# Performance work log

Measured on AMD Instinct MI355X. Metric: run time of the kernel, lower is better.

Reference implementation:

```python
import jax, jax.numpy as jnp
import numpy as np

NUM_HEADS = 12
QK_SCALE = 1.0
EPS = 1e-12  # torch.nn.functional.normalize default eps


def _l2norm(t):
    # matches torch F.normalize: x / max(||x||_2, eps) along last axis
    n = jnp.sqrt(jnp.sum(t * t, axis=-1, keepdims=True))
    return t / jnp.maximum(n, EPS)


def setup_inputs() -> dict:
    key = jax.random.key(0)
    k1, k2 = jax.random.split(key)
    B, N, dim = 8, 4096, 768
    x = jax.random.normal(k1, (B, N, 3 * dim), dtype=jnp.float32)
    temperature = jnp.ones((NUM_HEADS, 1, 1), dtype=jnp.float32)
    proj_w = jax.random.normal(k2, (dim, dim), dtype=jnp.float32) * (1.0 / np.sqrt(dim))
    proj_b = jnp.zeros((dim,), dtype=jnp.float32)
    return {"x": x, "temperature": temperature, "proj_w": proj_w, "proj_b": proj_b}


def reference(x, temperature, proj_w, proj_b):
    B, N, C3 = x.shape
    C = C3 // 3
    H = NUM_HEADS
    d = C // H
    # (B, N, 3, H, d) -> (3, B, H, N, d)
    qkv = x.reshape(B, N, 3, H, d).transpose(2, 0, 3, 1, 4)
    q, k, v = qkv[0], qkv[1], qkv[2]
    q = jnp.swapaxes(q, -2, -1) * QK_SCALE   # [B, H, d, N]
    v = jnp.swapaxes(v, -2, -1)              # [B, H, d, N]
    q = _l2norm(q)                           # normalize over tokens N
    k = _l2norm(k)                           # normalize over head dim d (k is [B,H,N,d])
    # cross-covariance attention over channels: [B, H, d, d]
    attn = jnp.einsum('bhdn,bhne->bhde', q, k) * temperature
    attn = jax.nn.softmax(attn, axis=-1)
    out = jnp.einsum('bhde,bhen->bhdn', attn, v)  # [B, H, d, N]
    out = out.transpose(0, 3, 1, 2).reshape(B, N, C)  # [B, N, C]
    out = out @ proj_w.T + proj_b
    return out
```

## Files before the change

kernel.cpp:

```cpp
#include <hip/hip_runtime.h>
#include <hip/hip_bf16.h>

#define BB 8
#define NN 4096
#define HH 12
#define CC 768
#define C3 2304

typedef float  f32x4  __attribute__((ext_vector_type(4)));
typedef __bf16 bf16x8 __attribute__((ext_vector_type(8)));
typedef __bf16 bf16x4 __attribute__((ext_vector_type(4)));

__device__ __forceinline__ void gload16(const void* g, void* l) {
  __builtin_amdgcn_global_load_lds((const __attribute__((address_space(1))) void*)g,
                                   (__attribute__((address_space(3))) void*)l, 16, 0, 0);
}

__global__ __launch_bounds__(256) void k1_logits(const float* __restrict__ x,
                                                 __bf16* __restrict__ vb,
                                                 float* __restrict__ Spart,
                                                 float* __restrict__ Qpart) {
  const int slice = blockIdx.x;
  const int h = blockIdx.y, b = blockIdx.z;
  const int tid = threadIdx.x;
  __shared__ __bf16 qT[2][64][40];
  __shared__ __bf16 kT[2][64][40];
  __shared__ float  qws[4][64];

  const int t   = tid >> 3;
  const int sub = tid & 7;
  const int w   = tid >> 6, lane = tid & 63;
  const int fr  = lane & 15, fk = lane >> 4;
  const int c0  = sub * 8;

  const float* qbase = x + (size_t)(b * NN + slice * 256) * C3 + h * 64 + c0;

  float qss8[8];
#pragma unroll
  for (int j = 0; j < 8; ++j) qss8[j] = 0.f;
  f32x4 acc[4];
#pragma unroll
  for (int tn = 0; tn < 4; ++tn) acc[tn] = (f32x4){0.f, 0.f, 0.f, 0.f};

  {
    const float* qp = qbase + (size_t)t * C3;
    const float4 q0 = *(const float4*)(qp);
    const float4 q1 = *(const float4*)(qp + 4);
    const float4 k0 = *(const float4*)(qp + 768);
    const float4 k1 = *(const float4*)(qp + 772);
    float ss = k0.x * k0.x + k0.y * k0.y + k0.z * k0.z + k0.w * k0.w +
               k1.x * k1.x + k1.y * k1.y + k1.z * k1.z + k1.w * k1.w;
    ss += __shfl_xor(ss, 1);
    ss += __shfl_xor(ss, 2);
    ss += __shfl_xor(ss, 4);
    const float inv = 1.0f / fmaxf(sqrtf(ss), 1e-12f);
    qT[0][c0 + 0][t] = (__bf16)q0.x; qT[0][c0 + 1][t] = (__bf16)q0.y;
    qT[0][c0 + 2][t] = (__bf16)q0.z; qT[0][c0 + 3][t] = (__bf16)q0.w;
    qT[0][c0 + 4][t] = (__bf16)q1.x; qT[0][c0 + 5][t] = (__bf16)q1.y;
    qT[0][c0 + 6][t] = (__bf16)q1.z; qT[0][c0 + 7][t] = (__bf16)q1.w;
    kT[0][c0 + 0][t] = (__bf16)(k0.x * inv); kT[0][c0 + 1][t] = (__bf16)(k0.y * inv);
    kT[0][c0 + 2][t] = (__bf16)(k0.z * inv); kT[0][c0 + 3][t] = (__bf16)(k0.w * inv);
    kT[0][c0 + 4][t] = (__bf16)(k1.x * inv); kT[0][c0 + 5][t] = (__bf16)(k1.y * inv);
    kT[0][c0 + 6][t] = (__bf16)(k1.z * inv); kT[0][c0 + 7][t] = (__bf16)(k1.w * inv);
    qss8[0] = fmaf(q0.x, q0.x, qss8[0]); qss8[1] = fmaf(q0.y, q0.y, qss8[1]);
    qss8[2] = fmaf(q0.z, q0.z, qss8[2]); qss8[3] = fmaf(q0.w, q0.w, qss8[3]);
    qss8[4] = fmaf(q1.x, q1.x, qss8[4]); qss8[5] = fmaf(q1.y, q1.y, qss8[5]);
    qss8[6] = fmaf(q1.z, q1.z, qss8[6]); qss8[7] = fmaf(q1.w, q1.w, qss8[7]);
  }
  __syncthreads();

#pragma unroll
  for (int step = 0; step < 8; ++step) {
    const int cur = step & 1;
    float4 q0, q1, k0, k1;
    if (step < 7) {
      const float* np = qbase + (size_t)((step + 1) * 32 + t) * C3;
      q0 = *(const float4*)(np);
      q1 = *(const float4*)(np + 4);
      k0 = *(const float4*)(np + 768);
      k1 = *(const float4*)(np + 772);
    }
    const bf16x8 afr = *(const bf16x8*)&qT[cur][w * 16 + fr][fk * 8];
    const bf16x8 b0 = *(const bf16x8*)&kT[cur][0 * 16 + fr][fk * 8];
    const bf16x8 b1 = *(const bf16x8*)&kT[cur][1 * 16 + fr][fk * 8];
    const bf16x8 b2 = *(const bf16x8*)&kT[cur][2 * 16 + fr][fk * 8];
    const bf16x8 b3 = *(const bf16x8*)&kT[cur][3 * 16 + fr][fk * 8];
    acc[0] = __builtin_amdgcn_mfma_f32_16x16x32_bf16(afr, b0, acc[0], 0, 0, 0);
    acc[1] = __builtin_amdgcn_mfma_f32_16x16x32_bf16(afr, b1, acc[1], 0, 0, 0);
    acc[2] = __builtin_amdgcn_mfma_f32_16x16x32_bf16(afr, b2, acc[2], 0, 0, 0);
    acc[3] = __builtin_amdgcn_mfma_f32_16x16x32_bf16(afr, b3, acc[3], 0, 0, 0);
    if (step < 7) {
      const int nxt = cur ^ 1;
      float ss = k0.x * k0.x + k0.y * k0.y + k0.z * k0.z + k0.w * k0.w +
                 k1.x * k1.x + k1.y * k1.y + k1.z * k1.z + k1.w * k1.w;
      ss += __shfl_xor(ss, 1);
      ss += __shfl_xor(ss, 2);
      ss += __shfl_xor(ss, 4);
      const float inv = 1.0f / fmaxf(sqrtf(ss), 1e-12f);
      qT[nxt][c0 + 0][t] = (__bf16)q0.x; qT[nxt][c0 + 1][t] = (__bf16)q0.y;
      qT[nxt][c0 + 2][t] = (__bf16)q0.z; qT[nxt][c0 + 3][t] = (__bf16)q0.w;
      qT[nxt][c0 + 4][t] = (__bf16)q1.x; qT[nxt][c0 + 5][t] = (__bf16)q1.y;
      qT[nxt][c0 + 6][t] = (__bf16)q1.z; qT[nxt][c0 + 7][t] = (__bf16)q1.w;
      kT[nxt][c0 + 0][t] = (__bf16)(k0.x * inv); kT[nxt][c0 + 1][t] = (__bf16)(k0.y * inv);
      kT[nxt][c0 + 2][t] = (__bf16)(k0.z * inv); kT[nxt][c0 + 3][t] = (__bf16)(k0.w * inv);
      kT[nxt][c0 + 4][t] = (__bf16)(k1.x * inv); kT[nxt][c0 + 5][t] = (__bf16)(k1.y * inv);
      kT[nxt][c0 + 6][t] = (__bf16)(k1.z * inv); kT[nxt][c0 + 7][t] = (__bf16)(k1.w * inv);
      qss8[0] = fmaf(q0.x, q0.x, qss8[0]); qss8[1] = fmaf(q0.y, q0.y, qss8[1]);
      qss8[2] = fmaf(q0.z, q0.z, qss8[2]); qss8[3] = fmaf(q0.w, q0.w, qss8[3]);
      qss8[4] = fmaf(q1.x, q1.x, qss8[4]); qss8[5] = fmaf(q1.y, q1.y, qss8[5]);
      qss8[6] = fmaf(q1.z, q1.z, qss8[6]); qss8[7] = fmaf(q1.w, q1.w, qss8[7]);
    }
    __syncthreads();
  }

  const int bh = b * HH + h;
  float* Sp = Spart + ((size_t)(slice * 96 + bh)) * 4096;
#pragma unroll
  for (int tn = 0; tn < 4; ++tn)
#pragma unroll
    for (int rr = 0; rr < 4; ++rr)
      Sp[(w * 16 + fk * 4 + rr) * 64 + tn * 16 + fr] = acc[tn][rr];

#pragma unroll
  for (int j = 0; j < 8; ++j) {
    float v = qss8[j];
    v += __shfl_xor(v, 8);
    v += __shfl_xor(v, 16);
    v += __shfl_xor(v, 32);
    if (lane < 8) qws[w][lane * 8 + j] = v;
  }
  __syncthreads();
  if (tid < 64) {
    const float qs = qws[0][tid] + qws[1][tid] + qws[2][tid] + qws[3][tid];
    Qpart[((size_t)(slice * 96 + bh)) * 64 + tid] = qs;
  }

  const float* vsrc = x + (size_t)(b * NN + slice * 256) * C3 + 1536 + h * 64 + c0;
  __bf16* vdst = vb + (size_t)(b * NN + slice * 256) * CC + h * 64 + c0;
#pragma unroll
  for (int r = 0; r < 8; ++r) {
    const size_t tok = (size_t)(r * 32 + t);
    const float4 v0 = *(const float4*)(vsrc + tok * C3);
    const float4 v1 = *(const float4*)(vsrc + tok * C3 + 4);
    bf16x8 vv;
    vv[0] = (__bf16)v0.x; vv[1] = (__bf16)v0.y; vv[2] = (__bf16)v0.z; vv[3] = (__bf16)v0.w;
    vv[4] = (__bf16)v1.x; vv[5] = (__bf16)v1.y; vv[6] = (__bf16)v1.z; vv[7] = (__bf16)v1.w;
    *(bf16x8*)(vdst + tok * CC) = vv;
  }
}

__global__ __launch_bounds__(512) void k2_softmax(const float* __restrict__ Spart,
                                                  const float* __restrict__ Qpart,
                                                  const float* __restrict__ temp,
                                                  float* __restrict__ attn) {
  const int h = blockIdx.x, b = blockIdx.y;
  const int tid = threadIdx.x;
  const int i = tid >> 3;
  const int g = tid & 7;
  const int bh = b * HH + h;
  float qs = 0.f;
#pragma unroll
  for (int s = 0; s < 16; ++s) qs += Qpart[((size_t)(s * 96 + bh)) * 64 + i];
  float v[8];
#pragma unroll
  for (int j = 0; j < 8; ++j) v[j] = 0.f;
#pragma unroll 4
  for (int s = 0; s < 16; ++s) {
    const float* Sp = Spart + ((size_t)(s * 96 + bh)) * 4096 + i * 64 + g * 8;
    const float4 t0 = *(const float4*)(Sp);
    const float4 t1 = *(const float4*)(Sp + 4);
    v[0] += t0.x; v[1] += t0.y; v[2] += t0.z; v[3] += t0.w;
    v[4] += t1.x; v[5] += t1.y; v[6] += t1.z; v[7] += t1.w;
  }
  const float rqs = 1.0f / fmaxf(sqrtf(qs), 1e-12f);
  const float tp  = temp[h] * rqs;
  float m = -3.4e38f;
#pragma unroll
  for (int j = 0; j < 8; ++j) { v[j] *= tp; m = fmaxf(m, v[j]); }
  m = fmaxf(m, __shfl_xor(m, 1));
  m = fmaxf(m, __shfl_xor(m, 2));
  m = fmaxf(m, __shfl_xor(m, 4));
  float s = 0.f;
#pragma unroll
  for (int j = 0; j < 8; ++j) { v[j] = __expf(v[j] - m); s += v[j]; }
  s += __shfl_xor(s, 1);
  s += __shfl_xor(s, 2);
  s += __shfl_xor(s, 4);
  const float inv = 1.0f / s;
  float* Ap = attn + (size_t)bh * 4096 + i * 64 + g * 8;
  float4 o0, o1;
  o0.x = v[0] * inv; o0.y = v[1] * inv; o0.z = v[2] * inv; o0.w = v[3] * inv;
  o1.x = v[4] * inv; o1.y = v[5] * inv; o1.z = v[6] * inv; o1.w = v[7] * inv;
  *(float4*)(Ap)     = o0;
  *(float4*)(Ap + 4) = o1;
}

__global__ __launch_bounds__(256) void k3_w2(const float* __restrict__ attn,
                                             const float* __restrict__ pw,
                                             __bf16* __restrict__ W2) {
  const int ct = blockIdx.x, h = blockIdx.y, b = blockIdx.z;
  const int co0 = ct * 64;
  __shared__ float pT[64][65];
  __shared__ float ab[64][64];
  const int tid = threadIdx.x;
  const int r = tid >> 2, c0 = (tid & 3) * 16;
  {
    const float* pp = pw + (size_t)(co0 + r) * CC + h * 64 + c0;
    const float4 p0 = *(const float4*)(pp + 0);
    const float4 p1 = *(const float4*)(pp + 4);
    const float4 p2 = *(const float4*)(pp + 8);
    const float4 p3 = *(const float4*)(pp + 12);
    const float* ap = attn + (size_t)(b * HH + h) * 4096 + r * 64 + c0;
    const float4 a0 = *(const float4*)(ap + 0);
    const float4 a1 = *(const float4*)(ap + 4);
    const float4 a2 = *(const float4*)(ap + 8);
    const float4 a3 = *(const float4*)(ap + 12);
    pT[c0 +  0][r] = p0.x; pT[c0 +  1][r] = p0.y; pT[c0 +  2][r] = p0.z; pT[c0 +  3][r] = p0.w;
    pT[c0 +  4][r] = p1.x; pT[c0 +  5][r] = p1.y; pT[c0 +  6][r] = p1.z; pT[c0 +  7][r] = p1.w;
    pT[c0 +  8][r] = p2.x; pT[c0 +  9][r] = p2.y; pT[c0 + 10][r] = p2.z; pT[c0 + 11][r] = p2.w;
    pT[c0 + 12][r] = p3.x; pT[c0 + 13][r] = p3.y; pT[c0 + 14][r] = p3.z; pT[c0 + 15][r] = p3.w;
    *(float4*)&ab[r][c0 + 0]  = a0;
    *(float4*)&ab[r][c0 + 4]  = a1;
    *(float4*)&ab[r][c0 + 8]  = a2;
    *(float4*)&ab[r][c0 + 12] = a3;
  }
  __syncthreads();
  const int col = tid & 63, jg = tid >> 6;
  float accJ[16];
#pragma unroll
  for (int c = 0; c < 16; ++c) accJ[c] = 0.f;
#pragma unroll 4
  for (int i = 0; i < 64; ++i) {
    const float p = pT[i][col];
    const float4* a4 = (const float4*)&ab[i][jg * 16];
    const float4 A0 = a4[0], A1 = a4[1], A2 = a4[2], A3 = a4[3];
    accJ[0]  = fmaf(p, A0.x, accJ[0]);  accJ[1]  = fmaf(p, A0.y, accJ[1]);
    accJ[2]  = fmaf(p, A0.z, accJ[2]);  accJ[3]  = fmaf(p, A0.w, accJ[3]);
    accJ[4]  = fmaf(p, A1.x, accJ[4]);  accJ[5]  = fmaf(p, A1.y, accJ[5]);
    accJ[6]  = fmaf(p, A1.z, accJ[6]);  accJ[7]  = fmaf(p, A1.w, accJ[7]);
    accJ[8]  = fmaf(p, A2.x, accJ[8]);  accJ[9]  = fmaf(p, A2.y, accJ[9]);
    accJ[10] = fmaf(p, A2.z, accJ[10]); accJ[11] = fmaf(p, A2.w, accJ[11]);
    accJ[12] = fmaf(p, A3.x, accJ[12]); accJ[13] = fmaf(p, A3.y, accJ[13]);
    accJ[14] = fmaf(p, A3.z, accJ[14]); accJ[15] = fmaf(p, A3.w, accJ[15]);
  }
  bf16x8 u0, u1;
#pragma unroll
  for (int c = 0; c < 8; ++c) { u0[c] = (__bf16)accJ[c]; u1[c] = (__bf16)accJ[8 + c]; }
  __bf16* wp = W2 + ((size_t)b * CC + co0 + col) * CC + h * 64 + jg * 16;
  *(bf16x8*)(wp)     = u0;
  *(bf16x8*)(wp + 8) = u1;
}

__global__ __launch_bounds__(256) void k4_gemm(const __bf16* __restrict__ vb,
                                               const __bf16* __restrict__ W2,
                                               const float* __restrict__ pb,
                                               float* __restrict__ out) {
  int id = blockIdx.x;
  const int bz = id / 192;
  const int rem = id - bz * 192;
  const int mg = rem / 48;
  const int idx = rem - mg * 48;
  const int nt = idx >> 3;
  const int mt = mg * 8 + (idx & 7);
  const int m0 = mt * 128, co0 = nt * 128;

  __shared__ __bf16 At[128][32];
  __shared__ __bf16 Bt[128][32];

  const int tid  = threadIdx.x;
  const int w    = tid >> 6, lane = tid & 63;
  const int wm   = w >> 1,   wn   = w & 1;
  const int fr   = lane & 15;
  const int fk   = lane >> 4;

  f32x4 acc[4][4];
#pragma unroll
  for (int tm = 0; tm < 4; ++tm)
#pragma unroll
    for (int tn = 0; tn < 4; ++tn) acc[tm][tn] = (f32x4){0.f, 0.f, 0.f, 0.f};

  const int srow = lane >> 2;
  const int scol = (lane & 3) * 8;
  const __bf16* Ag = vb + (size_t)(bz * NN + m0 + w * 32 + srow) * CC + scol;
  const __bf16* Bg = W2 + ((size_t)bz * CC + co0 + w * 32 + srow) * CC + scol;
  __bf16* lA0 = &At[w * 32][0];
  __bf16* lA1 = &At[w * 32 + 16][0];
  __bf16* lB0 = &Bt[w * 32][0];
  __bf16* lB1 = &Bt[w * 32 + 16][0];

  for (int kk = 0; kk < 24; ++kk) {
    const int kb = kk * 32;
    __syncthreads();
    gload16(Ag + kb,            lA0);
    gload16(Ag + 16 * CC + kb,  lA1);
    gload16(Bg + kb,            lB0);
    gload16(Bg + 16 * CC + kb,  lB1);
    __syncthreads();
    bf16x8 afr[4], bfr[4];
#pragma unroll
    for (int tm = 0; tm < 4; ++tm)
      afr[tm] = *(const bf16x8*)&At[wm * 64 + tm * 16 + fr][fk * 8];
#pragma unroll
    for (int tn = 0; tn < 4; ++tn)
      bfr[tn] = *(const bf16x8*)&Bt[wn * 64 + tn * 16 + fr][fk * 8];
#pragma unroll
    for (int tm = 0; tm < 4; ++tm)
#pragma unroll
      for (int tn = 0; tn < 4; ++tn)
        acc[tm][tn] = __builtin_amdgcn_mfma_f32_16x16x32_bf16(afr[tm], bfr[tn],
                                                              acc[tm][tn], 0, 0, 0);
  }

#pragma unroll
  for (int tn = 0; tn < 4; ++tn) {
    const int co = co0 + wn * 64 + tn * 16 + fr;
    const float bias = pb[co];
#pragma unroll
    for (int tm = 0; tm < 4; ++tm) {
#pragma unroll
      for (int rr = 0; rr < 4; ++rr) {
        const int row = m0 + wm * 64 + tm * 16 + fk * 4 + rr;
        out[(size_t)(bz * NN + row) * CC + co] = acc[tm][tn][rr] + bias;
      }
    }
  }
}

extern "C" void kernel_launch(void* const* d_in, const int* in_sizes, int n_in,
                              void* d_out, int out_size, void* d_ws, size_t ws_size,
                              hipStream_t stream) {
  const float* x    = (const float*)d_in[0];
  const float* temp = (const float*)d_in[1];
  const float* pw   = (const float*)d_in[2];
  const float* pb   = (const float*)d_in[3];
  float* out = (float*)d_out;
  char* ws = (char*)d_ws;

  float*  Spart = (float*)(ws);
  float*  Qpart = (float*)(ws + 25165824);
  float*  attn  = (float*)(ws + 25559040);
  __bf16* W2    = (__bf16*)(ws + 27131904);
  __bf16* vb    = (__bf16*)(ws + 36569088);

  hipLaunchKernelGGL(k1_logits,  dim3(16, 12, 8), dim3(256), 0, stream, x, vb, Spart, Qpart);
  hipLaunchKernelGGL(k2_softmax, dim3(12, 8),     dim3(512), 0, stream, Spart, Qpart, temp, attn);
  hipLaunchKernelGGL(k3_w2,      dim3(12, 12, 8), dim3(256), 0, stream, attn, pw, W2);
  hipLaunchKernelGGL(k4_gemm,    dim3(1536),      dim3(256), 0, stream, vb, W2, pb, out);
}
```

Baseline: 521.9 us.

## Fuse V fp32-to-bf16 conversion into GEMM A-tile load, drop vb buffer

Removes the V conversion pass from the logits kernel and the intermediate bf16 V buffer. The final GEMM now reads V directly from the fp32 input, converts it to bf16 in registers and stores it to LDS, with the next tile's loads issued early as register prefetch. The block index is also remapped so consecutive blocks land on different batches (an XCD-style swizzle). This saves a write and a re-read of the bf16 intermediate. In exchange the GEMM reads fp32 (twice the bytes) and in-kernel register staging replaces the async global-to-LDS path for A.

```diff
diff --git a/kernel.cpp b/kernel.cpp
--- a/kernel.cpp
+++ b/kernel.cpp
@@ -17,7 +17,6 @@
 }
 
 __global__ __launch_bounds__(256) void k1_logits(const float* __restrict__ x,
-                                                 __bf16* __restrict__ vb,
                                                  float* __restrict__ Spart,
                                                  float* __restrict__ Qpart) {
   const int slice = blockIdx.x;
@@ -134,19 +133,6 @@
     const float qs = qws[0][tid] + qws[1][tid] + qws[2][tid] + qws[3][tid];
     Qpart[((size_t)(slice * 96 + bh)) * 64 + tid] = qs;
   }
-
-  const float* vsrc = x + (size_t)(b * NN + slice * 256) * C3 + 1536 + h * 64 + c0;
-  __bf16* vdst = vb + (size_t)(b * NN + slice * 256) * CC + h * 64 + c0;
-#pragma unroll
-  for (int r = 0; r < 8; ++r) {
-    const size_t tok = (size_t)(r * 32 + t);
-    const float4 v0 = *(const float4*)(vsrc + tok * C3);
-    const float4 v1 = *(const float4*)(vsrc + tok * C3 + 4);
-    bf16x8 vv;
-    vv[0] = (__bf16)v0.x; vv[1] = (__bf16)v0.y; vv[2] = (__bf16)v0.z; vv[3] = (__bf16)v0.w;
-    vv[4] = (__bf16)v1.x; vv[5] = (__bf16)v1.y; vv[6] = (__bf16)v1.z; vv[7] = (__bf16)v1.w;
-    *(bf16x8*)(vdst + tok * CC) = vv;
-  }
 }
 
 __global__ __launch_bounds__(512) void k2_softmax(const float* __restrict__ Spart,
@@ -251,11 +237,12 @@
   *(bf16x8*)(wp + 8) = u1;
 }
 
-__global__ __launch_bounds__(256) void k4_gemm(const __bf16* __restrict__ vb,
+__global__ __launch_bounds__(256) void k4_gemm(const float* __restrict__ x,
                                                const __bf16* __restrict__ W2,
                                                const float* __restrict__ pb,
                                                float* __restrict__ out) {
-  int id = blockIdx.x;
+  const int id0 = blockIdx.x;
+  const int id = (id0 & 7) * 192 + (id0 >> 3);
   const int bz = id / 192;
   const int rem = id - bz * 192;
   const int mg = rem / 48;
@@ -281,20 +268,38 @@
 
   const int srow = lane >> 2;
   const int scol = (lane & 3) * 8;
-  const __bf16* Ag = vb + (size_t)(bz * NN + m0 + w * 32 + srow) * CC + scol;
   const __bf16* Bg = W2 + ((size_t)bz * CC + co0 + w * 32 + srow) * CC + scol;
-  __bf16* lA0 = &At[w * 32][0];
-  __bf16* lA1 = &At[w * 32 + 16][0];
   __bf16* lB0 = &Bt[w * 32][0];
   __bf16* lB1 = &Bt[w * 32 + 16][0];
+
+  const int arow = tid >> 1;
+  const int ah   = (tid & 1) * 16;
+  const float* Ax = x + (size_t)(bz * NN + m0 + arow) * C3 + 1536 + ah;
+
+  float4 a0 = *(const float4*)(Ax + 0);
+  float4 a1 = *(const float4*)(Ax + 4);
+  float4 a2 = *(const float4*)(Ax + 8);
+  float4 a3 = *(const float4*)(Ax + 12);
 
   for (int kk = 0; kk < 24; ++kk) {
     const int kb = kk * 32;
     __syncthreads();
-    gload16(Ag + kb,            lA0);
-    gload16(Ag + 16 * CC + kb,  lA1);
     gload16(Bg + kb,            lB0);
     gload16(Bg + 16 * CC + kb,  lB1);
+    bf16x8 u0, u1;
+    u0[0] = (__bf16)a0.x; u0[1] = (__bf16)a0.y; u0[2] = (__bf16)a0.z; u0[3] = (__bf16)a0.w;
+    u0[4] = (__bf16)a1.x; u0[5] = (__bf16)a1.y; u0[6] = (__bf16)a1.z; u0[7] = (__bf16)a1.w;
+    u1[0] = (__bf16)a2.x; u1[1] = (__bf16)a2.y; u1[2] = (__bf16)a2.z; u1[3] = (__bf16)a2.w;
+    u1[4] = (__bf16)a3.x; u1[5] = (__bf16)a3.y; u1[6] = (__bf16)a3.z; u1[7] = (__bf16)a3.w;
+    *(bf16x8*)&At[arow][ah]     = u0;
+    *(bf16x8*)&At[arow][ah + 8] = u1;
+    if (kk < 23) {
+      const float* nx = Ax + kb + 32;
+      a0 = *(const float4*)(nx + 0);
+      a1 = *(const float4*)(nx + 4);
+      a2 = *(const float4*)(nx + 8);
+      a3 = *(const float4*)(nx + 12);
+    }
     __syncthreads();
     bf16x8 afr[4], bfr[4];
 #pragma unroll
@@ -340,10 +345,9 @@
   float*  Qpart = (float*)(ws + 25165824);
   float*  attn  = (float*)(ws + 25559040);
   __bf16* W2    = (__bf16*)(ws + 27131904);
-  __bf16* vb    = (__bf16*)(ws + 36569088);
-
-  hipLaunchKernelGGL(k1_logits,  dim3(16, 12, 8), dim3(256), 0, stream, x, vb, Spart, Qpart);
+
+  hipLaunchKernelGGL(k1_logits,  dim3(16, 12, 8), dim3(256), 0, stream, x, Spart, Qpart);
   hipLaunchKernelGGL(k2_softmax, dim3(12, 8),     dim3(512), 0, stream, Spart, Qpart, temp, attn);
   hipLaunchKernelGGL(k3_w2,      dim3(12, 12, 8), dim3(256), 0, stream, attn, pw, W2);
-  hipLaunchKernelGGL(k4_gemm,    dim3(1536),      dim3(256), 0, stream, vb, W2, pb, out);
-}
+  hipLaunchKernelGGL(k4_gemm,    dim3(1536),      dim3(256), 0, stream, x, W2, pb, out);
+}
```

Measured after the change: 533.5 us. +2.2%, slower.

## Load Q fragments directly into registers and swizzle packed K stores in LDS

Applied to the files above, without the earlier changes.

The Q operand of the logits MFMA is now read straight from global memory into each lane's A-fragment registers, which drops the Q transpose through LDS and the q sum-of-squares reduction through shared memory. K is reorganised so each thread normalises two tokens and writes packed bf16 pairs into an XOR-swizzled LDS layout, aiming to cut bank conflicts and the number of LDS stores. The trade-off is that Q is now fetched with scalar strided global loads (8 per step per lane) instead of float4 loads, which may coalesce worse. The step loop is also no longer fully unrolled.

```diff
diff --git a/kernel.cpp b/kernel.cpp
--- a/kernel.cpp
+++ b/kernel.cpp
@@ -14,6 +14,12 @@
 __device__ __forceinline__ void gload16(const void* g, void* l) {
   __builtin_amdgcn_global_load_lds((const __attribute__((address_space(1))) void*)g,
                                    (__attribute__((address_space(3))) void*)l, 16, 0, 0);
+}
+
+__device__ __forceinline__ unsigned int pk2(float a, float b) {
+  union { __bf16 h[2]; unsigned int u; } z;
+  z.h[0] = (__bf16)a; z.h[1] = (__bf16)b;
+  return z.u;
 }
 
 __global__ __launch_bounds__(256) void k1_logits(const float* __restrict__ x,
@@ -23,92 +29,96 @@
   const int slice = blockIdx.x;
   const int h = blockIdx.y, b = blockIdx.z;
   const int tid = threadIdx.x;
-  __shared__ __bf16 qT[2][64][40];
   __shared__ __bf16 kT[2][64][40];
-  __shared__ float  qws[4][64];
-
-  const int t   = tid >> 3;
-  const int sub = tid & 7;
-  const int w   = tid >> 6, lane = tid & 63;
-  const int fr  = lane & 15, fk = lane >> 4;
-  const int c0  = sub * 8;
-
-  const float* qbase = x + (size_t)(b * NN + slice * 256) * C3 + h * 64 + c0;
-
-  float qss8[8];
-#pragma unroll
-  for (int j = 0; j < 8; ++j) qss8[j] = 0.f;
+
+  const int w = tid >> 6, lane = tid & 63;
+  const int fr = lane & 15, fk = lane >> 4;
+  const int tp = tid >> 4;
+  const int cs = tid & 15;
+
+  const size_t rowbase = (size_t)(b * NN + slice * 256) * C3 + h * 64;
+  const float* qp = x + rowbase + w * 16 + fr;
+  const float* kp = x + rowbase + 768 + cs * 4;
+
+  const int wblk = ((w ^ (cs & 3)) << 4) + (tp & 3) * 4;
+  const int rblk = (fk ^ (fr >> 2)) << 4;
+
+  float qss = 0.f;
   f32x4 acc[4];
 #pragma unroll
   for (int tn = 0; tn < 4; ++tn) acc[tn] = (f32x4){0.f, 0.f, 0.f, 0.f};
 
+  bf16x8 afr;
   {
-    const float* qp = qbase + (size_t)t * C3;
-    const float4 q0 = *(const float4*)(qp);
-    const float4 q1 = *(const float4*)(qp + 4);
-    const float4 k0 = *(const float4*)(qp + 768);
-    const float4 k1 = *(const float4*)(qp + 772);
-    float ss = k0.x * k0.x + k0.y * k0.y + k0.z * k0.z + k0.w * k0.w +
-               k1.x * k1.x + k1.y * k1.y + k1.z * k1.z + k1.w * k1.w;
-    ss += __shfl_xor(ss, 1);
-    ss += __shfl_xor(ss, 2);
-    ss += __shfl_xor(ss, 4);
-    const float inv = 1.0f / fmaxf(sqrtf(ss), 1e-12f);
-    qT[0][c0 + 0][t] = (__bf16)q0.x; qT[0][c0 + 1][t] = (__bf16)q0.y;
-    qT[0][c0 + 2][t] = (__bf16)q0.z; qT[0][c0 + 3][t] = (__bf16)q0.w;
-    qT[0][c0 + 4][t] = (__bf16)q1.x; qT[0][c0 + 5][t] = (__bf16)q1.y;
-    qT[0][c0 + 6][t] = (__bf16)q1.z; qT[0][c0 + 7][t] = (__bf16)q1.w;
-    kT[0][c0 + 0][t] = (__bf16)(k0.x * inv); kT[0][c0 + 1][t] = (__bf16)(k0.y * inv);
-    kT[0][c0 + 2][t] = (__bf16)(k0.z * inv); kT[0][c0 + 3][t] = (__bf16)(k0.w * inv);
-    kT[0][c0 + 4][t] = (__bf16)(k1.x * inv); kT[0][c0 + 5][t] = (__bf16)(k1.y * inv);
-    kT[0][c0 + 6][t] = (__bf16)(k1.z * inv); kT[0][c0 + 7][t] = (__bf16)(k1.w * inv);
-    qss8[0] = fmaf(q0.x, q0.x, qss8[0]); qss8[1] = fmaf(q0.y, q0.y, qss8[1]);
-    qss8[2] = fmaf(q0.z, q0.z, qss8[2]); qss8[3] = fmaf(q0.w, q0.w, qss8[3]);
-    qss8[4] = fmaf(q1.x, q1.x, qss8[4]); qss8[5] = fmaf(q1.y, q1.y, qss8[5]);
-    qss8[6] = fmaf(q1.z, q1.z, qss8[6]); qss8[7] = fmaf(q1.w, q1.w, qss8[7]);
+    const int tb = fk * 8;
+    const float a0 = qp[(tb + 0) * C3], a1 = qp[(tb + 1) * C3];
+    const float a2 = qp[(tb + 2) * C3], a3 = qp[(tb + 3) * C3];
+    const float a4 = qp[(tb + 4) * C3], a5 = qp[(tb + 5) * C3];
+    const float a6 = qp[(tb + 6) * C3], a7 = qp[(tb + 7) * C3];
+    const float4 kv0 = *(const float4*)(kp + (size_t)(2 * tp) * C3);
+    const float4 kv1 = *(const float4*)(kp + (size_t)(2 * tp + 1) * C3);
+    float s0 = kv0.x * kv0.x + kv0.y * kv0.y + kv0.z * kv0.z + kv0.w * kv0.w;
+    float s1 = kv1.x * kv1.x + kv1.y * kv1.y + kv1.z * kv1.z + kv1.w * kv1.w;
+    s0 += __shfl_xor(s0, 1); s1 += __shfl_xor(s1, 1);
+    s0 += __shfl_xor(s0, 2); s1 += __shfl_xor(s1, 2);
+    s0 += __shfl_xor(s0, 4); s1 += __shfl_xor(s1, 4);
+    s0 += __shfl_xor(s0, 8); s1 += __shfl_xor(s1, 8);
+    const float i0 = 1.0f / fmaxf(sqrtf(s0), 1e-12f);
+    const float i1 = 1.0f / fmaxf(sqrtf(s1), 1e-12f);
+    char* kbz = (char*)&kT[0][0][0];
+    *(unsigned int*)(kbz + (cs * 4 + 0) * 80 + wblk) = pk2(kv0.x * i0, kv1.x * i1);
+    *(unsigned int*)(kbz + (cs * 4 + 1) * 80 + wblk) = pk2(kv0.y * i0, kv1.y * i1);
+    *(unsigned int*)(kbz + (cs * 4 + 2) * 80 + wblk) = pk2(kv0.z * i0, kv1.z * i1);
+    *(unsigned int*)(kbz + (cs * 4 + 3) * 80 + wblk) = pk2(kv0.w * i0, kv1.w * i1);
+    qss = a0 * a0 + a1 * a1 + a2 * a2 + a3 * a3 +
+          a4 * a4 + a5 * a5 + a6 * a6 + a7 * a7;
+    afr[0] = (__bf16)a0; afr[1] = (__bf16)a1; afr[2] = (__bf16)a2; afr[3] = (__bf16)a3;
+    afr[4] = (__bf16)a4; afr[5] = (__bf16)a5; afr[6] = (__bf16)a6; afr[7] = (__bf16)a7;
   }
   __syncthreads();
 
-#pragma unroll
   for (int step = 0; step < 8; ++step) {
     const int cur = step & 1;
-    float4 q0, q1, k0, k1;
+    float n0, n1, n2, n3, n4, n5, n6, n7;
+    float4 m0, m1;
     if (step < 7) {
-      const float* np = qbase + (size_t)((step + 1) * 32 + t) * C3;
-      q0 = *(const float4*)(np);
-      q1 = *(const float4*)(np + 4);
-      k0 = *(const float4*)(np + 768);
-      k1 = *(const float4*)(np + 772);
+      const int tb = (step + 1) * 32 + fk * 8;
+      n0 = qp[(tb + 0) * C3]; n1 = qp[(tb + 1) * C3];
+      n2 = qp[(tb + 2) * C3]; n3 = qp[(tb + 3) * C3];
+      n4 = qp[(tb + 4) * C3]; n5 = qp[(tb + 5) * C3];
+      n6 = qp[(tb + 6) * C3]; n7 = qp[(tb + 7) * C3];
+      m0 = *(const float4*)(kp + (size_t)((step + 1) * 32 + 2 * tp) * C3);
+      m1 = *(const float4*)(kp + (size_t)((step + 1) * 32 + 2 * tp + 1) * C3);
     }
-    const bf16x8 afr = *(const bf16x8*)&qT[cur][w * 16 + fr][fk * 8];
-    const bf16x8 b0 = *(const bf16x8*)&kT[cur][0 * 16 + fr][fk * 8];
-    const bf16x8 b1 = *(const bf16x8*)&kT[cur][1 * 16 + fr][fk * 8];
-    const bf16x8 b2 = *(const bf16x8*)&kT[cur][2 * 16 + fr][fk * 8];
-    const bf16x8 b3 = *(const bf16x8*)&kT[cur][3 * 16 + fr][fk * 8];
-    acc[0] = __builtin_amdgcn_mfma_f32_16x16x32_bf16(afr, b0, acc[0], 0, 0, 0);
-    acc[1] = __builtin_amdgcn_mfma_f32_16x16x32_bf16(afr, b1, acc[1], 0, 0, 0);
-    acc[2] = __builtin_amdgcn_mfma_f32_16x16x32_bf16(afr, b2, acc[2], 0, 0, 0);
-    acc[3] = __builtin_amdgcn_mfma_f32_16x16x32_bf16(afr, b3, acc[3], 0, 0, 0);
+    {
+      const char* kbz = (const char*)&kT[cur][0][0];
+      const bf16x8 b0 = *(const bf16x8*)(kbz + (0  + fr) * 80 + rblk);
+      const bf16x8 b1 = *(const bf16x8*)(kbz + (16 + fr) * 80 + rblk);
+      const bf16x8 b2 = *(const bf16x8*)(kbz + (32 + fr) * 80 + rblk);
+      const bf16x8 b3 = *(const bf16x8*)(kbz + (48 + fr) * 80 + rblk);
+      acc[0] = __builtin_amdgcn_mfma_f32_16x16x32_bf16(afr, b0, acc[0], 0, 0, 0);
+      acc[1] = __builtin_amdgcn_mfma_f32_16x16x32_bf16(afr, b1, acc[1], 0, 0, 0);
+      acc[2] = __builtin_amdgcn_mfma_f32_16x16x32_bf16(afr, b2, acc[2], 0, 0, 0);
+      acc[3] = __builtin_amdgcn_mfma_f32_16x16x32_bf16(afr, b3, acc[3], 0, 0, 0);
+    }
     if (step < 7) {
-      const int nxt = cur ^ 1;
-      float ss = k0.x * k0.x + k0.y * k0.y + k0.z * k0.z + k0.w * k0.w +
-                 k1.x * k1.x + k1.y * k1.y + k1.z * k1.z + k1.w * k1.w;
-      ss += __shfl_xor(ss, 1);
-      ss += __shfl_xor(ss, 2);
-      ss += __shfl_xor(ss, 4);
-      const float inv = 1.0f / fmaxf(sqrtf(ss), 1e-12f);
-      qT[nxt][c0 + 0][t] = (__bf16)q0.x; qT[nxt][c0 + 1][t] = (__bf16)q0.y;
-      qT[nxt][c0 + 2][t] = (__bf16)q0.z; qT[nxt][c0 + 3][t] = (__bf16)q0.w;
-      qT[nxt][c0 + 4][t] = (__bf16)q1.x; qT[nxt][c0 + 5][t] = (__bf16)q1.y;
-      qT[nxt][c0 + 6][t] = (__bf16)q1.z; qT[nxt][c0 + 7][t] = (__bf16)q1.w;
-      kT[nxt][c0 + 0][t] = (__bf16)(k0.x * inv); kT[nxt][c0 + 1][t] = (__bf16)(k0.y * inv);
-      kT[nxt][c0 + 2][t] = (__bf16)(k0.z * inv); kT[nxt][c0 + 3][t] = (__bf16)(k0.w * inv);
-      kT[nxt][c0 + 4][t] = (__bf16)(k1.x * inv); kT[nxt][c0 + 5][t] = (__bf16)(k1.y * inv);
-      kT[nxt][c0 + 6][t] = (__bf16)(k1.z * inv); kT[nxt][c0 + 7][t] = (__bf16)(k1.w * inv);
-      qss8[0] = fmaf(q0.x, q0.x, qss8[0]); qss8[1] = fmaf(q0.y, q0.y, qss8[1]);
-      qss8[2] = fmaf(q0.z, q0.z, qss8[2]); qss8[3] = fmaf(q0.w, q0.w, qss8[3]);
-      qss8[4] = fmaf(q1.x, q1.x, qss8[4]); qss8[5] = fmaf(q1.y, q1.y, qss8[5]);
-      qss8[6] = fmaf(q1.z, q1.z, qss8[6]); qss8[7] = fmaf(q1.w, q1.w, qss8[7]);
+      float s0 = m0.x * m0.x + m0.y * m0.y + m0.z * m0.z + m0.w * m0.w;
+      float s1 = m1.x * m1.x + m1.y * m1.y + m1.z * m1.z + m1.w * m1.w;
+      s0 += __shfl_xor(s0, 1); s1 += __shfl_xor(s1, 1);
+      s0 += __shfl_xor(s0, 2); s1 += __shfl_xor(s1, 2);
+      s0 += __shfl_xor(s0, 4); s1 += __shfl_xor(s1, 4);
+      s0 += __shfl_xor(s0, 8); s1 += __shfl_xor(s1, 8);
+      const float i0 = 1.0f / fmaxf(sqrtf(s0), 1e-12f);
+      const float i1 = 1.0f / fmaxf(sqrtf(s1), 1e-12f);
+      char* kbz = (char*)&kT[cur ^ 1][0][0];
+      *(unsigned int*)(kbz + (cs * 4 + 0) * 80 + wblk) = pk2(m0.x * i0, m1.x * i1);
+      *(unsigned int*)(kbz + (cs * 4 + 1) * 80 + wblk) = pk2(m0.y * i0, m1.y * i1);
+      *(unsigned int*)(kbz + (cs * 4 + 2) * 80 + wblk) = pk2(m0.z * i0, m1.z * i1);
+      *(unsigned int*)(kbz + (cs * 4 + 3) * 80 + wblk) = pk2(m0.w * i0, m1.w * i1);
+      qss += n0 * n0 + n1 * n1 + n2 * n2 + n3 * n3 +
+             n4 * n4 + n5 * n5 + n6 * n6 + n7 * n7;
+      afr[0] = (__bf16)n0; afr[1] = (__bf16)n1; afr[2] = (__bf16)n2; afr[3] = (__bf16)n3;
+      afr[4] = (__bf16)n4; afr[5] = (__bf16)n5; afr[6] = (__bf16)n6; afr[7] = (__bf16)n7;
     }
     __syncthreads();
   }
@@ -121,22 +131,17 @@
     for (int rr = 0; rr < 4; ++rr)
       Sp[(w * 16 + fk * 4 + rr) * 64 + tn * 16 + fr] = acc[tn][rr];
 
-#pragma unroll
-  for (int j = 0; j < 8; ++j) {
-    float v = qss8[j];
-    v += __shfl_xor(v, 8);
+  {
+    float v = qss;
     v += __shfl_xor(v, 16);
     v += __shfl_xor(v, 32);
-    if (lane < 8) qws[w][lane * 8 + j] = v;
-  }
-  __syncthreads();
-  if (tid < 64) {
-    const float qs = qws[0][tid] + qws[1][tid] + qws[2][tid] + qws[3][tid];
-    Qpart[((size_t)(slice * 96 + bh)) * 64 + tid] = qs;
-  }
-
-  const float* vsrc = x + (size_t)(b * NN + slice * 256) * C3 + 1536 + h * 64 + c0;
-  __bf16* vdst = vb + (size_t)(b * NN + slice * 256) * CC + h * 64 + c0;
+    if (lane < 16)
+      Qpart[((size_t)(slice * 96 + bh)) * 64 + w * 16 + lane] = v;
+  }
+
+  const int t = tid >> 3, sub = tid & 7, c0v = sub * 8;
+  const float* vsrc = x + (size_t)(b * NN + slice * 256) * C3 + 1536 + h * 64 + c0v;
+  __bf16* vdst = vb + (size_t)(b * NN + slice * 256) * CC + h * 64 + c0v;
 #pragma unroll
   for (int r = 0; r < 8; ++r) {
     const size_t tok = (size_t)(r * 32 + t);
```

Measured after the change: 521.7 us. No clear change (-0.0%).
